# Kernel optimization log

Hardware: AMD Instinct MI355X
Metric: run time of the kernel (lower is better)

The kernel has to match this reference:

```python
import jax, jax.numpy as jnp
import numpy as np


def setup_inputs() -> dict:
    key = jax.random.key(0)
    ks = jax.random.split(key, 6)
    B, N, S, D, A = 32, 12, 512, 256, 96
    return {
        "value": jax.random.normal(ks[0], (B, N, S, D), dtype=jnp.float32),
        "emb": jax.random.normal(ks[1], (N, S, A), dtype=jnp.float32),
        "Wqk": jax.random.normal(ks[2], (A, D), dtype=jnp.float32) * (A ** -0.5),
        "bqk": jax.random.normal(ks[3], (D,), dtype=jnp.float32) * 0.02,
        "Wv": jax.random.normal(ks[4], (D, D), dtype=jnp.float32) * (D ** -0.5),
        "bv": jax.random.normal(ks[5], (D,), dtype=jnp.float32) * 0.02,
    }


def reference(value, emb, Wqk, bqk, Wv, bv):
    # qk: [n, s, d] -- query and key share the same projection FC_Q_K
    qk = emb @ Wqk + bqk
    v = value @ Wv + bv                      # [b, n, s, d]
    q = jax.nn.softmax(qk, axis=-1)          # softmax over d (last dim of query)
    k = jax.nn.softmax(qk.swapaxes(-1, -2), axis=-1)  # [n, d, s], softmax over s
    # key @ value: [n, d, s] x [b, n, s, e] -> [b, n, d, e] (broadcast over b)
    kv = jnp.einsum('nds,bnse->bnde', k, v)
    # query @ kv: [n, s, d] x [b, n, d, e] -> [b, n, s, e]
    out = jnp.einsum('nsd,bnde->bnse', q, kv)
    return out
```

## Files before the change

kernel.cpp:

```cpp
#include <hip/hip_runtime.h>
#include <hip/hip_bf16.h>

#define B_ 32
#define N_ 12
#define S_ 512
#define D_ 256
#define A_ 96

typedef __attribute__((ext_vector_type(8))) short short8;
typedef __attribute__((ext_vector_type(4))) float float4v;

static __device__ __forceinline__ ushort f2bf(float f) {
  union { float f; unsigned u; } a;
  a.f = f;
  return (ushort)((a.u + 0x7FFFu + ((a.u >> 16) & 1u)) >> 16);
}

__global__ __launch_bounds__(256) void k_qk_softmax_q(
    const float* __restrict__ emb, const float* __restrict__ Wqk,
    const float* __restrict__ bqk, float* __restrict__ qk,
    ushort* __restrict__ qb) {
  const int blk = blockIdx.x;
  const int tid = threadIdx.x;
  const int d = tid;
  const int wv = tid >> 6, lane = tid & 63;
  __shared__ float seT[A_][8];
  __shared__ float redm[8][4], reds[8][4];
  const float* ebase = emb + (size_t)blk * 8 * A_;
  for (int k = tid; k < 8 * A_; k += 256) {
    int r = k / A_, a = k - r * A_;
    seT[a][r] = ebase[k];
  }
  __syncthreads();
  float bq = bqk[d];
  float acc[8];
#pragma unroll
  for (int r = 0; r < 8; ++r) acc[r] = bq;
#pragma unroll 8
  for (int a = 0; a < A_; ++a) {
    float w = Wqk[a * D_ + d];
    float4 lo = *(const float4*)(&seT[a][0]);
    float4 hi = *(const float4*)(&seT[a][4]);
    acc[0] = fmaf(lo.x, w, acc[0]);
    acc[1] = fmaf(lo.y, w, acc[1]);
    acc[2] = fmaf(lo.z, w, acc[2]);
    acc[3] = fmaf(lo.w, w, acc[3]);
    acc[4] = fmaf(hi.x, w, acc[4]);
    acc[5] = fmaf(hi.y, w, acc[5]);
    acc[6] = fmaf(hi.z, w, acc[6]);
    acc[7] = fmaf(hi.w, w, acc[7]);
  }
  const size_t obase = (size_t)blk * 8 * D_ + d;
#pragma unroll
  for (int r = 0; r < 8; ++r) qk[obase + r * D_] = acc[r];
  float m[8];
#pragma unroll
  for (int r = 0; r < 8; ++r) {
    m[r] = acc[r];
    for (int off = 32; off; off >>= 1) m[r] = fmaxf(m[r], __shfl_xor(m[r], off));
  }
  if (lane == 0) {
#pragma unroll
    for (int r = 0; r < 8; ++r) redm[r][wv] = m[r];
  }
  __syncthreads();
  float e[8], s[8];
#pragma unroll
  for (int r = 0; r < 8; ++r) {
    float mm = fmaxf(fmaxf(redm[r][0], redm[r][1]),
                     fmaxf(redm[r][2], redm[r][3]));
    e[r] = __expf(acc[r] - mm);
    s[r] = e[r];
    for (int off = 32; off; off >>= 1) s[r] += __shfl_xor(s[r], off);
  }
  if (lane == 0) {
#pragma unroll
    for (int r = 0; r < 8; ++r) reds[r][wv] = s[r];
  }
  __syncthreads();
#pragma unroll
  for (int r = 0; r < 8; ++r) {
    float sum = reds[r][0] + reds[r][1] + reds[r][2] + reds[r][3];
    qb[obase + r * D_] = f2bf(e[r] / sum);
  }
}

__global__ __launch_bounds__(256) void k_softmax_kT(
    const float* __restrict__ qk, ushort* __restrict__ kTb) {
  const int dc = blockIdx.x * 16;
  const int n = blockIdx.y;
  const int tid = threadIdx.x;
  __shared__ float t[16][514];
  const float* base = qk + (size_t)n * S_ * D_ + dc;
#pragma unroll
  for (int it = 0; it < 8; ++it) {
    int id = it * 256 + tid;
    int d4 = id & 3, s = id >> 2;
    float4 v = *(const float4*)(base + (size_t)s * D_ + 4 * d4);
    t[4 * d4 + 0][s] = v.x;
    t[4 * d4 + 1][s] = v.y;
    t[4 * d4 + 2][s] = v.z;
    t[4 * d4 + 3][s] = v.w;
  }
  __syncthreads();
  const int d = tid >> 4, sg = tid & 15;
  float vv[32];
  float m = -1e30f;
#pragma unroll
  for (int k = 0; k < 32; ++k) {
    vv[k] = t[d][sg + 16 * k];
    m = fmaxf(m, vv[k]);
  }
  for (int off = 1; off < 16; off <<= 1) m = fmaxf(m, __shfl_xor(m, off));
  float sum = 0.0f;
#pragma unroll
  for (int k = 0; k < 32; ++k) {
    vv[k] = __expf(vv[k] - m);
    sum += vv[k];
  }
  for (int off = 1; off < 16; off <<= 1) sum += __shfl_xor(sum, off);
  float inv = 1.0f / sum;
  const size_t ob = ((size_t)n * D_ + dc + d) * S_;
#pragma unroll
  for (int k = 0; k < 32; ++k) kTb[ob + sg + 16 * k] = f2bf(vv[k] * inv);
}

__global__ __launch_bounds__(256) void k_wvt(const float* __restrict__ Wv,
                                             ushort* __restrict__ WvT) {
  int c = blockIdx.x, e = threadIdx.x;
  WvT[c * D_ + e] = f2bf(Wv[e * D_ + c]);
}

__global__ __launch_bounds__(256) void k_kv0(
    const ushort* __restrict__ kTb, const float* __restrict__ value,
    ushort* __restrict__ kv0) {
  const int eb = blockIdx.x * 64;
  const int bz = blockIdx.y;
  const int n = bz % N_;
  const int tid = threadIdx.x;
  const int l = tid & 63, w = tid >> 6;
  const int lane16 = l & 15, quad = l >> 4;

  __shared__ ushort ldsV[64 * 72];
  __shared__ ushort ldsK[256 * 72];

  float4v acc[4][4];
#pragma unroll
  for (int i = 0; i < 4; ++i)
#pragma unroll
    for (int j = 0; j < 4; ++j) acc[i][j] = (float4v)0.0f;

  const ushort* kTbase = kTb + (size_t)n * D_ * S_;
  const float* vbase = value + (size_t)bz * S_ * D_ + eb;

  for (int sc = 0; sc < S_; sc += 64) {
    __syncthreads();
#pragma unroll
    for (int it = 0; it < 8; ++it) {
      int id = it * 256 + tid;
      int rd = id >> 3, cc = (id & 7) * 8;
      *(uint4*)(&ldsK[rd * 72 + cc]) =
          *(const uint4*)(kTbase + rd * S_ + sc + cc);
    }
#pragma unroll
    for (int it = 0; it < 4; ++it) {
      int id = it * 256 + tid;
      int e = id & 63, sq = id >> 6;
      float f0 = vbase[(sc + 4 * sq + 0) * D_ + e];
      float f1 = vbase[(sc + 4 * sq + 1) * D_ + e];
      float f2 = vbase[(sc + 4 * sq + 2) * D_ + e];
      float f3 = vbase[(sc + 4 * sq + 3) * D_ + e];
      ushort4 p;
      p.x = f2bf(f0);
      p.y = f2bf(f1);
      p.z = f2bf(f2);
      p.w = f2bf(f3);
      *(ushort4*)(&ldsV[e * 72 + 4 * sq]) = p;
    }
    __syncthreads();
#pragma unroll
    for (int kc = 0; kc < 64; kc += 32) {
      int ko = kc + quad * 8;
      short8 a[4], b[4];
#pragma unroll
      for (int i = 0; i < 4; ++i)
        a[i] = *(const short8*)(&ldsV[(i * 16 + lane16) * 72 + ko]);
#pragma unroll
      for (int j = 0; j < 4; ++j)
        b[j] = *(const short8*)(&ldsK[(w * 64 + j * 16 + lane16) * 72 + ko]);
#pragma unroll
      for (int i = 0; i < 4; ++i)
#pragma unroll
        for (int j = 0; j < 4; ++j)
          acc[i][j] = __builtin_amdgcn_mfma_f32_16x16x32_bf16(a[i], b[j],
                                                              acc[i][j], 0, 0, 0);
    }
  }
  ushort* obase = kv0 + (size_t)bz * D_ * D_;
#pragma unroll
  for (int i = 0; i < 4; ++i) {
#pragma unroll
    for (int j = 0; j < 4; ++j) {
      int d = w * 64 + j * 16 + lane16;
      int e0 = eb + i * 16 + quad * 4;
      ushort4 p;
      p.x = f2bf(acc[i][j][0]);
      p.y = f2bf(acc[i][j][1]);
      p.z = f2bf(acc[i][j][2]);
      p.w = f2bf(acc[i][j][3]);
      *(ushort4*)(obase + d * D_ + e0) = p;
    }
  }
}

__global__ __launch_bounds__(256) void k_kvw_inplace(
    ushort* kv0, const ushort* __restrict__ WvT,
    const float* __restrict__ bv) {
  const int qd = blockIdx.x;
  const int bz = blockIdx.y;
  const int tid = threadIdx.x;
  const int l = tid & 63, w = tid >> 6;
  const int lane16 = l & 15, quad = l >> 4;

  __shared__ ushort ldsA[64 * 72];
  __shared__ ushort ldsB[256 * 72];

  float4v acc[4][4];
#pragma unroll
  for (int i = 0; i < 4; ++i)
#pragma unroll
    for (int j = 0; j < 4; ++j) acc[i][j] = (float4v)0.0f;

  ushort* base = kv0 + (size_t)bz * (D_ * D_) + qd * (64 * D_);

  for (int ec = 0; ec < D_; ec += 64) {
    __syncthreads();
#pragma unroll
    for (int it = 0; it < 2; ++it) {
      int id = it * 256 + tid;
      int rd = id >> 3, cc = (id & 7) * 8;
      *(uint4*)(&ldsA[rd * 72 + cc]) =
          *(const uint4*)(base + rd * D_ + ec + cc);
    }
#pragma unroll
    for (int it = 0; it < 8; ++it) {
      int id = it * 256 + tid;
      int rd = id >> 3, cc = (id & 7) * 8;
      *(uint4*)(&ldsB[rd * 72 + cc]) =
          *(const uint4*)(WvT + rd * D_ + ec + cc);
    }
    __syncthreads();
#pragma unroll
    for (int kc = 0; kc < 64; kc += 32) {
      int ko = kc + quad * 8;
      short8 a[4], b[4];
#pragma unroll
      for (int i = 0; i < 4; ++i)
        a[i] = *(const short8*)(&ldsA[(i * 16 + lane16) * 72 + ko]);
#pragma unroll
      for (int j = 0; j < 4; ++j)
        b[j] = *(const short8*)(&ldsB[(w * 64 + j * 16 + lane16) * 72 + ko]);
#pragma unroll
      for (int i = 0; i < 4; ++i)
#pragma unroll
        for (int j = 0; j < 4; ++j)
          acc[i][j] = __builtin_amdgcn_mfma_f32_16x16x32_bf16(a[i], b[j],
                                                              acc[i][j], 0, 0, 0);
    }
  }
#pragma unroll
  for (int i = 0; i < 4; ++i) {
#pragma unroll
    for (int j = 0; j < 4; ++j) {
      int c = w * 64 + j * 16 + lane16;
      int d0 = i * 16 + quad * 4;
      float bvc = bv[c];
      ushort4 p;
      p.x = f2bf(acc[i][j][0] + bvc);
      p.y = f2bf(acc[i][j][1] + bvc);
      p.z = f2bf(acc[i][j][2] + bvc);
      p.w = f2bf(acc[i][j][3] + bvc);
      *(ushort4*)(base + c * 64 + d0) = p;
    }
  }
}

__global__ __launch_bounds__(256) void k_out(
    const ushort* __restrict__ qb, const ushort* __restrict__ kvw,
    float* __restrict__ out) {
  const int bx = blockIdx.x;
  const int by = blockIdx.y;
  const int bz = blockIdx.z;
  const int n = bz % N_;
  const int tid = threadIdx.x;
  const int l = tid & 63, w = tid >> 6;
  const int wm = w & 1, wn = w >> 1;
  const int lane16 = l & 15, quad = l >> 4;

  __shared__ ushort ldsA[128 * 72];
  __shared__ ushort ldsB[128 * 72];

  float4v acc[4][4];
#pragma unroll
  for (int i = 0; i < 4; ++i)
#pragma unroll
    for (int j = 0; j < 4; ++j) acc[i][j] = (float4v)0.0f;

  const ushort* abase = qb + (size_t)n * S_ * D_ + bx * 128 * D_;
  const ushort* bbase = kvw + (size_t)bz * D_ * D_;

  for (int dc = 0; dc < D_; dc += 64) {
    __syncthreads();
#pragma unroll
    for (int it = 0; it < 4; ++it) {
      int id = it * 256 + tid;
      int rd = id >> 3, cc = (id & 7) * 8;
      *(uint4*)(&ldsA[rd * 72 + cc]) =
          *(const uint4*)(abase + rd * D_ + dc + cc);
    }
#pragma unroll
    for (int it = 0; it < 4; ++it) {
      int id = it * 256 + tid;
      int rd = id >> 3, cc = (id & 7) * 8;
      *(uint4*)(&ldsB[rd * 72 + cc]) =
          *(const uint4*)(bbase + (dc >> 6) * 16384 + (by * 128 + rd) * 64 +
                          cc);
    }
    __syncthreads();
#pragma unroll
    for (int kc = 0; kc < 64; kc += 32) {
      int ko = kc + quad * 8;
      short8 a[4], b[4];
#pragma unroll
      for (int i = 0; i < 4; ++i)
        a[i] = *(const short8*)(&ldsA[(wm * 64 + i * 16 + lane16) * 72 + ko]);
#pragma unroll
      for (int j = 0; j < 4; ++j)
        b[j] = *(const short8*)(&ldsB[(wn * 64 + j * 16 + lane16) * 72 + ko]);
#pragma unroll
      for (int i = 0; i < 4; ++i)
#pragma unroll
        for (int j = 0; j < 4; ++j)
          acc[i][j] = __builtin_amdgcn_mfma_f32_16x16x32_bf16(a[i], b[j],
                                                              acc[i][j], 0, 0, 0);
    }
  }
  float* obase = out + (size_t)bz * S_ * D_;
#pragma unroll
  for (int i = 0; i < 4; ++i) {
#pragma unroll
    for (int j = 0; j < 4; ++j) {
      int s0 = bx * 128 + wm * 64 + i * 16 + quad * 4;
      int c = by * 128 + wn * 64 + j * 16 + lane16;
#pragma unroll
      for (int r = 0; r < 4; ++r)
        obase[(s0 + r) * D_ + c] = acc[i][j][r];
    }
  }
}

extern "C" void kernel_launch(void* const* d_in, const int* in_sizes, int n_in,
                              void* d_out, int out_size, void* d_ws,
                              size_t ws_size, hipStream_t stream) {
  const float* value = (const float*)d_in[0];
  const float* emb   = (const float*)d_in[1];
  const float* Wqk   = (const float*)d_in[2];
  const float* bqk   = (const float*)d_in[3];
  const float* Wv    = (const float*)d_in[4];
  const float* bv    = (const float*)d_in[5];
  float* out = (float*)d_out;

  char* ws = (char*)d_ws;
  float*  qk  = (float*)ws;
  ushort* qb  = (ushort*)(ws + 6291456);
  ushort* kTb = (ushort*)(ws + 9437184);
  ushort* kv0 = (ushort*)(ws + 12582912);
  ushort* WvT = (ushort*)(ws + 62914560);

  k_qk_softmax_q<<<dim3(N_ * S_ / 8), 256, 0, stream>>>(emb, Wqk, bqk, qk, qb);
  k_softmax_kT<<<dim3(16, N_), 256, 0, stream>>>(qk, kTb);
  k_wvt<<<dim3(D_), 256, 0, stream>>>(Wv, WvT);
  k_kv0<<<dim3(4, B_ * N_), 256, 0, stream>>>(kTb, value, kv0);
  k_kvw_inplace<<<dim3(4, B_ * N_), 256, 0, stream>>>(kv0, WvT, bv);
  k_out<<<dim3(4, 2, B_ * N_), 256, 0, stream>>>(qb, kv0, out);
}
```

Baseline: 445.6 us.

## Fuse kv0 and Wv projection kernels into one LDS-resident kernel; remap block order

Merges the K^T·V GEMM and the following Wv projection into a single 512-thread kernel. Each block computes a 128x256 slice of kv in LDS and immediately multiplies it by WvT, so the intermediate kv0 no longer round-trips through global memory and one launch is removed. Each block now reads the full 256-wide value rows, and k_out's grid is flattened with a swizzled block index to improve cache locality across XCDs. The risk is about 108KB of LDS per block, which lowers occupancy.

```diff
diff --git a/kernel.cpp b/kernel.cpp
--- a/kernel.cpp
+++ b/kernel.cpp
@@ -131,18 +131,25 @@
   WvT[c * D_ + e] = f2bf(Wv[e * D_ + c]);
 }
 
-__global__ __launch_bounds__(256) void k_kv0(
+__global__ __launch_bounds__(512) void k_kv_fused(
     const ushort* __restrict__ kTb, const float* __restrict__ value,
-    ushort* __restrict__ kv0) {
-  const int eb = blockIdx.x * 64;
-  const int bz = blockIdx.y;
+    const ushort* __restrict__ WvT, const float* __restrict__ bv,
+    ushort* __restrict__ kvw) {
+  const int f = blockIdx.x;
+  const int wk = (f & 7) * 96 + (f >> 3);
+  const int h = wk & 1;
+  const int bz = wk >> 1;
   const int n = bz % N_;
   const int tid = threadIdx.x;
   const int l = tid & 63, w = tid >> 6;
+  const int wd = w & 1, we = w >> 1;
   const int lane16 = l & 15, quad = l >> 4;
 
-  __shared__ ushort ldsV[64 * 72];
-  __shared__ ushort ldsK[256 * 72];
+  __shared__ ushort smem[54272];
+  ushort* ldsK = smem;
+  ushort* ldsV = smem + 9216;
+  ushort* ldsKV = smem;
+  ushort* ldsW = smem + 35840;
 
   float4v acc[4][4];
 #pragma unroll
@@ -150,22 +157,22 @@
 #pragma unroll
     for (int j = 0; j < 4; ++j) acc[i][j] = (float4v)0.0f;
 
-  const ushort* kTbase = kTb + (size_t)n * D_ * S_;
-  const float* vbase = value + (size_t)bz * S_ * D_ + eb;
+  const ushort* kTbase = kTb + ((size_t)(n * D_ + h * 128)) * S_;
+  const float* vbase = value + (size_t)bz * S_ * D_;
 
   for (int sc = 0; sc < S_; sc += 64) {
     __syncthreads();
 #pragma unroll
-    for (int it = 0; it < 8; ++it) {
-      int id = it * 256 + tid;
+    for (int it = 0; it < 2; ++it) {
+      int id = it * 512 + tid;
       int rd = id >> 3, cc = (id & 7) * 8;
       *(uint4*)(&ldsK[rd * 72 + cc]) =
           *(const uint4*)(kTbase + rd * S_ + sc + cc);
     }
 #pragma unroll
-    for (int it = 0; it < 4; ++it) {
-      int id = it * 256 + tid;
-      int e = id & 63, sq = id >> 6;
+    for (int it = 0; it < 8; ++it) {
+      int id = it * 512 + tid;
+      int e = id & 255, sq = id >> 8;
       float f0 = vbase[(sc + 4 * sq + 0) * D_ + e];
       float f1 = vbase[(sc + 4 * sq + 1) * D_ + e];
       float f2 = vbase[(sc + 4 * sq + 2) * D_ + e];
@@ -184,10 +191,10 @@
       short8 a[4], b[4];
 #pragma unroll
       for (int i = 0; i < 4; ++i)
-        a[i] = *(const short8*)(&ldsV[(i * 16 + lane16) * 72 + ko]);
+        a[i] = *(const short8*)(&ldsV[(we * 64 + i * 16 + lane16) * 72 + ko]);
 #pragma unroll
       for (int j = 0; j < 4; ++j)
-        b[j] = *(const short8*)(&ldsK[(w * 64 + j * 16 + lane16) * 72 + ko]);
+        b[j] = *(const short8*)(&ldsK[(wd * 64 + j * 16 + lane16) * 72 + ko]);
 #pragma unroll
       for (int i = 0; i < 4; ++i)
 #pragma unroll
@@ -196,58 +203,35 @@
                                                               acc[i][j], 0, 0, 0);
     }
   }
-  ushort* obase = kv0 + (size_t)bz * D_ * D_;
+  __syncthreads();
 #pragma unroll
   for (int i = 0; i < 4; ++i) {
 #pragma unroll
     for (int j = 0; j < 4; ++j) {
-      int d = w * 64 + j * 16 + lane16;
-      int e0 = eb + i * 16 + quad * 4;
+      int dl = wd * 64 + j * 16 + lane16;
+      int e0 = we * 64 + i * 16 + quad * 4;
       ushort4 p;
       p.x = f2bf(acc[i][j][0]);
       p.y = f2bf(acc[i][j][1]);
       p.z = f2bf(acc[i][j][2]);
       p.w = f2bf(acc[i][j][3]);
-      *(ushort4*)(obase + d * D_ + e0) = p;
-    }
-  }
-}
-
-__global__ __launch_bounds__(256) void k_kvw_inplace(
-    ushort* kv0, const ushort* __restrict__ WvT,
-    const float* __restrict__ bv) {
-  const int qd = blockIdx.x;
-  const int bz = blockIdx.y;
-  const int tid = threadIdx.x;
-  const int l = tid & 63, w = tid >> 6;
-  const int lane16 = l & 15, quad = l >> 4;
-
-  __shared__ ushort ldsA[64 * 72];
-  __shared__ ushort ldsB[256 * 72];
-
-  float4v acc[4][4];
+      *(ushort4*)(&ldsKV[dl * 280 + e0]) = p;
+    }
+  }
+
+  float4v acc2[4][4];
 #pragma unroll
   for (int i = 0; i < 4; ++i)
 #pragma unroll
-    for (int j = 0; j < 4; ++j) acc[i][j] = (float4v)0.0f;
-
-  ushort* base = kv0 + (size_t)bz * (D_ * D_) + qd * (64 * D_);
+    for (int j = 0; j < 4; ++j) acc2[i][j] = (float4v)0.0f;
 
   for (int ec = 0; ec < D_; ec += 64) {
     __syncthreads();
 #pragma unroll
-    for (int it = 0; it < 2; ++it) {
-      int id = it * 256 + tid;
+    for (int it = 0; it < 4; ++it) {
+      int id = it * 512 + tid;
       int rd = id >> 3, cc = (id & 7) * 8;
-      *(uint4*)(&ldsA[rd * 72 + cc]) =
-          *(const uint4*)(base + rd * D_ + ec + cc);
-    }
-#pragma unroll
-    for (int it = 0; it < 8; ++it) {
-      int id = it * 256 + tid;
-      int rd = id >> 3, cc = (id & 7) * 8;
-      *(uint4*)(&ldsB[rd * 72 + cc]) =
-          *(const uint4*)(WvT + rd * D_ + ec + cc);
+      *(uint4*)(&ldsW[rd * 72 + cc]) = *(const uint4*)(WvT + rd * D_ + ec + cc);
     }
     __syncthreads();
 #pragma unroll
@@ -256,31 +240,33 @@
       short8 a[4], b[4];
 #pragma unroll
       for (int i = 0; i < 4; ++i)
-        a[i] = *(const short8*)(&ldsA[(i * 16 + lane16) * 72 + ko]);
+        a[i] = *(const short8*)(&ldsKV[(wd * 64 + i * 16 + lane16) * 280 + ec +
+                                       ko]);
 #pragma unroll
       for (int j = 0; j < 4; ++j)
-        b[j] = *(const short8*)(&ldsB[(w * 64 + j * 16 + lane16) * 72 + ko]);
+        b[j] = *(const short8*)(&ldsW[(we * 64 + j * 16 + lane16) * 72 + ko]);
 #pragma unroll
       for (int i = 0; i < 4; ++i)
 #pragma unroll
         for (int j = 0; j < 4; ++j)
-          acc[i][j] = __builtin_amdgcn_mfma_f32_16x16x32_bf16(a[i], b[j],
-                                                              acc[i][j], 0, 0, 0);
-    }
-  }
+          acc2[i][j] = __builtin_amdgcn_mfma_f32_16x16x32_bf16(a[i], b[j],
+                                                               acc2[i][j], 0, 0, 0);
+    }
+  }
+  ushort* obase = kvw + (size_t)bz * (D_ * D_) + (h * 2 + wd) * 16384;
 #pragma unroll
   for (int i = 0; i < 4; ++i) {
 #pragma unroll
     for (int j = 0; j < 4; ++j) {
-      int c = w * 64 + j * 16 + lane16;
-      int d0 = i * 16 + quad * 4;
+      int c = we * 64 + j * 16 + lane16;
+      int d6 = i * 16 + quad * 4;
       float bvc = bv[c];
       ushort4 p;
-      p.x = f2bf(acc[i][j][0] + bvc);
-      p.y = f2bf(acc[i][j][1] + bvc);
-      p.z = f2bf(acc[i][j][2] + bvc);
-      p.w = f2bf(acc[i][j][3] + bvc);
-      *(ushort4*)(base + c * 64 + d0) = p;
+      p.x = f2bf(acc2[i][j][0] + bvc);
+      p.y = f2bf(acc2[i][j][1] + bvc);
+      p.z = f2bf(acc2[i][j][2] + bvc);
+      p.w = f2bf(acc2[i][j][3] + bvc);
+      *(ushort4*)(obase + c * 64 + d6) = p;
     }
   }
 }
@@ -288,9 +274,11 @@
 __global__ __launch_bounds__(256) void k_out(
     const ushort* __restrict__ qb, const ushort* __restrict__ kvw,
     float* __restrict__ out) {
-  const int bx = blockIdx.x;
-  const int by = blockIdx.y;
-  const int bz = blockIdx.z;
+  const int f = blockIdx.x;
+  const int wk = (f & 7) * 384 + (f >> 3);
+  const int bx = wk & 3;
+  const int by = (wk >> 2) & 1;
+  const int bz = wk >> 3;
   const int n = bz % N_;
   const int tid = threadIdx.x;
   const int l = tid & 63, w = tid >> 6;
@@ -374,13 +362,12 @@
   float*  qk  = (float*)ws;
   ushort* qb  = (ushort*)(ws + 6291456);
   ushort* kTb = (ushort*)(ws + 9437184);
-  ushort* kv0 = (ushort*)(ws + 12582912);
+  ushort* kvw = (ushort*)(ws + 12582912);
   ushort* WvT = (ushort*)(ws + 62914560);
 
   k_qk_softmax_q<<<dim3(N_ * S_ / 8), 256, 0, stream>>>(emb, Wqk, bqk, qk, qb);
   k_softmax_kT<<<dim3(16, N_), 256, 0, stream>>>(qk, kTb);
   k_wvt<<<dim3(D_), 256, 0, stream>>>(Wv, WvT);
-  k_kv0<<<dim3(4, B_ * N_), 256, 0, stream>>>(kTb, value, kv0);
-  k_kvw_inplace<<<dim3(4, B_ * N_), 256, 0, stream>>>(kv0, WvT, bv);
-  k_out<<<dim3(4, 2, B_ * N_), 256, 0, stream>>>(qb, kv0, out);
-}
+  k_kv_fused<<<dim3(2 * B_ * N_), 512, 0, stream>>>(kTb, value, WvT, bv, kvw);
+  k_out<<<dim3(4 * 2 * B_ * N_), 256, 0, stream>>>(qb, kvw, out);
+}
```

After: 439.8 us. About the same (-1.3%).

## Restructure kv0 kernel with double-buffered V, direct K loads, and XCD-aware block remap

Applied to the files above, without the earlier changes.

The k_kv0 kernel now uses 512 threads, each wave owning 32 d-rows. The K^T operand is read straight from global memory instead of being staged in LDS, and V is double-buffered in a swizzled LDS layout. The next V tile is prefetched into registers during the MFMA loop, so only one barrier per iteration remains. Both k_kv0 and k_out flatten their grid and remap block indices so consecutive work lands on the same XCD for better L2 locality, at the cost of more global traffic for K and a larger block footprint.

```diff
diff --git a/kernel.cpp b/kernel.cpp
--- a/kernel.cpp
+++ b/kernel.cpp
@@ -131,84 +131,96 @@
   WvT[c * D_ + e] = f2bf(Wv[e * D_ + c]);
 }
 
-__global__ __launch_bounds__(256) void k_kv0(
+__global__ __launch_bounds__(512) void k_kv0(
     const ushort* __restrict__ kTb, const float* __restrict__ value,
     ushort* __restrict__ kv0) {
-  const int eb = blockIdx.x * 64;
-  const int bz = blockIdx.y;
+  const int f = blockIdx.x;
+  const int wk = (f & 7) * 192 + (f >> 3);
+  const int eq = wk & 3;
+  const int bz = wk >> 2;
   const int n = bz % N_;
   const int tid = threadIdx.x;
   const int l = tid & 63, w = tid >> 6;
   const int lane16 = l & 15, quad = l >> 4;
 
-  __shared__ ushort ldsV[64 * 72];
-  __shared__ ushort ldsK[256 * 72];
-
-  float4v acc[4][4];
+  __shared__ ushort ldsV[2][64 * 72];
+
+  const int se = tid & 63;
+  const int sch = tid >> 6;
+  const int schs = (sch ^ ((se >> 3) & 7)) << 3;
+  const float* vbase = value + (size_t)bz * S_ * D_ + eq * 64 + se;
+  const ushort* kTbase = kTb + (size_t)n * D_ * S_ + (w * 32) * S_;
+
+  float4v acc[4][2];
 #pragma unroll
   for (int i = 0; i < 4; ++i)
 #pragma unroll
-    for (int j = 0; j < 4; ++j) acc[i][j] = (float4v)0.0f;
-
-  const ushort* kTbase = kTb + (size_t)n * D_ * S_;
-  const float* vbase = value + (size_t)bz * S_ * D_ + eb;
-
+    for (int j = 0; j < 2; ++j) acc[i][j] = (float4v)0.0f;
+
+  union Pack { ushort u[8]; uint4 v; };
+
+  {
+    float f0[8];
+#pragma unroll
+    for (int t = 0; t < 8; ++t) f0[t] = vbase[(size_t)(sch * 8 + t) * D_];
+    Pack pk;
+#pragma unroll
+    for (int t = 0; t < 8; ++t) pk.u[t] = f2bf(f0[t]);
+    *(uint4*)(&ldsV[0][se * 72 + schs]) = pk.v;
+  }
+
+  int p = 0;
   for (int sc = 0; sc < S_; sc += 64) {
     __syncthreads();
-#pragma unroll
-    for (int it = 0; it < 8; ++it) {
-      int id = it * 256 + tid;
-      int rd = id >> 3, cc = (id & 7) * 8;
-      *(uint4*)(&ldsK[rd * 72 + cc]) =
-          *(const uint4*)(kTbase + rd * S_ + sc + cc);
-    }
-#pragma unroll
-    for (int it = 0; it < 4; ++it) {
-      int id = it * 256 + tid;
-      int e = id & 63, sq = id >> 6;
-      float f0 = vbase[(sc + 4 * sq + 0) * D_ + e];
-      float f1 = vbase[(sc + 4 * sq + 1) * D_ + e];
-      float f2 = vbase[(sc + 4 * sq + 2) * D_ + e];
-      float f3 = vbase[(sc + 4 * sq + 3) * D_ + e];
-      ushort4 p;
-      p.x = f2bf(f0);
-      p.y = f2bf(f1);
-      p.z = f2bf(f2);
-      p.w = f2bf(f3);
-      *(ushort4*)(&ldsV[e * 72 + 4 * sq]) = p;
-    }
-    __syncthreads();
+    float fs[8];
+    const bool more = (sc + 64 < S_);
+    if (more) {
+#pragma unroll
+      for (int t = 0; t < 8; ++t)
+        fs[t] = vbase[(size_t)(sc + 64 + sch * 8 + t) * D_];
+    }
 #pragma unroll
     for (int kc = 0; kc < 64; kc += 32) {
-      int ko = kc + quad * 8;
-      short8 a[4], b[4];
+      const int ko = kc + quad * 8;
+      const int chr = ko >> 3;
+      short8 a[4], b[2];
+#pragma unroll
+      for (int i = 0; i < 4; ++i) {
+        int er = i * 16 + lane16;
+        a[i] = *(const short8*)(
+            &ldsV[p][er * 72 + ((chr ^ ((er >> 3) & 7)) << 3)]);
+      }
+#pragma unroll
+      for (int j = 0; j < 2; ++j)
+        b[j] = *(const short8*)(kTbase + (j * 16 + lane16) * S_ + sc + ko);
 #pragma unroll
       for (int i = 0; i < 4; ++i)
-        a[i] = *(const short8*)(&ldsV[(i * 16 + lane16) * 72 + ko]);
-#pragma unroll
-      for (int j = 0; j < 4; ++j)
-        b[j] = *(const short8*)(&ldsK[(w * 64 + j * 16 + lane16) * 72 + ko]);
-#pragma unroll
-      for (int i = 0; i < 4; ++i)
-#pragma unroll
-        for (int j = 0; j < 4; ++j)
+#pragma unroll
+        for (int j = 0; j < 2; ++j)
           acc[i][j] = __builtin_amdgcn_mfma_f32_16x16x32_bf16(a[i], b[j],
                                                               acc[i][j], 0, 0, 0);
     }
+    if (more) {
+      Pack pk;
+#pragma unroll
+      for (int t = 0; t < 8; ++t) pk.u[t] = f2bf(fs[t]);
+      *(uint4*)(&ldsV[p ^ 1][se * 72 + schs]) = pk.v;
+    }
+    p ^= 1;
   }
   ushort* obase = kv0 + (size_t)bz * D_ * D_;
 #pragma unroll
   for (int i = 0; i < 4; ++i) {
 #pragma unroll
-    for (int j = 0; j < 4; ++j) {
-      int d = w * 64 + j * 16 + lane16;
-      int e0 = eb + i * 16 + quad * 4;
-      ushort4 p;
-      p.x = f2bf(acc[i][j][0]);
-      p.y = f2bf(acc[i][j][1]);
-      p.z = f2bf(acc[i][j][2]);
-      p.w = f2bf(acc[i][j][3]);
-      *(ushort4*)(obase + d * D_ + e0) = p;
+    for (int j = 0; j < 2; ++j) {
+      int d = w * 32 + j * 16 + lane16;
+      int e0 = eq * 64 + i * 16 + quad * 4;
+      ushort4 pk;
+      pk.x = f2bf(acc[i][j][0]);
+      pk.y = f2bf(acc[i][j][1]);
+      pk.z = f2bf(acc[i][j][2]);
+      pk.w = f2bf(acc[i][j][3]);
+      *(ushort4*)(obase + d * D_ + e0) = pk;
     }
   }
 }
@@ -288,9 +300,11 @@
 __global__ __launch_bounds__(256) void k_out(
     const ushort* __restrict__ qb, const ushort* __restrict__ kvw,
     float* __restrict__ out) {
-  const int bx = blockIdx.x;
-  const int by = blockIdx.y;
-  const int bz = blockIdx.z;
+  const int f = blockIdx.x;
+  const int wk = (f & 7) * 384 + (f >> 3);
+  const int bx = wk & 3;
+  const int by = (wk >> 2) & 1;
+  const int bz = wk >> 3;
   const int n = bz % N_;
   const int tid = threadIdx.x;
   const int l = tid & 63, w = tid >> 6;
@@ -380,7 +394,7 @@
   k_qk_softmax_q<<<dim3(N_ * S_ / 8), 256, 0, stream>>>(emb, Wqk, bqk, qk, qb);
   k_softmax_kT<<<dim3(16, N_), 256, 0, stream>>>(qk, kTb);
   k_wvt<<<dim3(D_), 256, 0, stream>>>(Wv, WvT);
-  k_kv0<<<dim3(4, B_ * N_), 256, 0, stream>>>(kTb, value, kv0);
+  k_kv0<<<dim3(4 * B_ * N_), 512, 0, stream>>>(kTb, value, kv0);
   k_kvw_inplace<<<dim3(4, B_ * N_), 256, 0, stream>>>(kv0, WvT, bv);
-  k_out<<<dim3(4, 2, B_ * N_), 256, 0, stream>>>(qb, kv0, out);
-}
+  k_out<<<dim3(4 * 2 * B_ * N_), 256, 0, stream>>>(qb, kv0, out);
+}
```

Result: no change. 449.8 us (+1.0%).
